# Kernel optimization log

Hardware: AMD Instinct MI355X
Metric: run time of the kernel (lower is better)

The kernel has to match this reference:

```python
import jax, jax.numpy as jnp
import numpy as np

MARGIN = 2.0


def setup_inputs() -> dict:
    key = jax.random.key(0)
    k1, k2 = jax.random.split(key)
    B, D, NUM_CLASSES = 8192, 128, 100
    features = jax.random.normal(k1, (B, D), dtype=jnp.float32)
    labels = jax.random.randint(k2, (B,), 0, NUM_CLASSES, dtype=jnp.int64)
    return {"features": features, "labels": labels}


def reference(features, labels):
    # Vectorized form of the O(B^2) nested-loop contrastive loss.
    B = features.shape[0]
    sq = jnp.sum(features * features, axis=-1)                      # [B]
    # squared pairwise L2 distances via the gram matrix
    d2 = sq[:, None] + sq[None, :] - 2.0 * (features @ features.T)  # [B, B]
    d2 = jnp.maximum(d2, 0.0)

    off_diag = ~jnp.eye(B, dtype=bool)
    same = labels[:, None] == labels[None, :]
    pos_mask = same & off_diag
    neg_mask = (~same) & off_diag

    # positive pairs contribute squared distance
    pos_loss = jnp.sum(jnp.where(pos_mask, d2, 0.0))

    # negative pairs contribute clamp(margin - dist, 0)^2; guard sqrt(0) grads
    d = jnp.sqrt(jnp.where(neg_mask, d2, 1.0))
    hinge = jnp.maximum(MARGIN - d, 0.0)
    neg_loss = jnp.sum(jnp.where(neg_mask, hinge * hinge, 0.0))

    pos_count = jnp.sum(pos_mask)
    total_pairs = jnp.asarray(B * (B - 1), dtype=d2.dtype)
    loss = pos_loss + neg_loss
    # original divides only when positive_pairs > 0
    return jnp.where(pos_count > 0, loss / total_pairs, loss)
```

## Files before the change

### kernel.cpp

```cpp
#include <hip/hip_runtime.h>
#include <hip/hip_bf16.h>


#define BN 8192
#define DD 128
#define NTILES 64
#define NBLOCKS (NTILES * (NTILES + 1) / 2)
#define SQ 26.0f
#define INV_S2 (1.0 / (26.0 * 26.0))
#define INV_S2F (1.0f / (26.0f * 26.0f))
#define D2I_HINGE 2704
#define NCLS 100
#define IMIN ((int)0x80000000)

typedef __attribute__((ext_vector_type(4))) int i32x4;

__global__ __launch_bounds__(256) void prep_kernel(const float* __restrict__ f,
        const int* __restrict__ labels, char* __restrict__ fbp,
        int* __restrict__ normv, int* __restrict__ csum_g) {
    const int tid = threadIdx.x;
    const int p = blockIdx.x;
    __shared__ __align__(16) char ls[16][144];
    __shared__ int lslab[16];

    if (tid < 16) lslab[tid] = labels[p * 16 + tid];

    const int r = tid >> 4;
    const int c = (tid & 15) * 8;
    const float* src = f + ((size_t)p * 16 + r) * DD + c;
    float4 a = *(const float4*)src;
    float4 b = *(const float4*)(src + 4);
    float rv[8] = {a.x, a.y, a.z, a.w, b.x, b.y, b.z, b.w};
    int s = 0;
#pragma unroll
    for (int j = 0; j < 8; j++) {
        int q = __float2int_rn(fminf(fmaxf(rv[j] * SQ, -127.f), 127.f));
        ls[r][c + j] = (char)q;
        s += q * q;
    }
#pragma unroll
    for (int off = 8; off > 0; off >>= 1) s += __shfl_down(s, off, 16);
    if ((tid & 15) == 0) normv[p * 16 + r] = s;
    __syncthreads();

    if (tid < 128) {
        const int ks = tid >> 6, lane = tid & 63;
        const int l15 = lane & 15, quad = lane >> 4;
        i32x4 pack = *(const i32x4*)&ls[l15][ks * 64 + quad * 16];
        *(i32x4*)(fbp + ((size_t)(p * 2 + ks) * 64 + lane) * 16) = pack;
    }

#pragma unroll
    for (int i = 0; i < 8; i++) {
        const int k = tid + i * 256;
        const int row = k >> 7, d = k & 127;
        const int q = (int)(signed char)ls[row][d];
        atomicAdd(&csum_g[lslab[row] * DD + d], q);
    }
}

__global__ __launch_bounds__(256) void pair_kernel(
        const char* __restrict__ fbp, const int* __restrict__ normv,
        const int* __restrict__ labels, float* __restrict__ partial) {
    const int t = blockIdx.x;
    int by = (int)((sqrtf(8.f * (float)t + 1.f) - 1.f) * 0.5f);
    while ((by + 1) * (by + 2) / 2 <= t) by++;
    while (by * (by + 1) / 2 > t) by--;
    const int bx = t - by * (by + 1) / 2;
    const bool diag = (bx == by);

    const int tid = threadIdx.x;
    const int wave = tid >> 6, lane = tid & 63;
    const int wx = wave & 1, wy = wave >> 1;
    const int i0 = bx * 128 + wy * 64;
    const int j0 = by * 128 + wx * 64;
    const int ip = i0 >> 4, jp = j0 >> 4;
    const int l15 = lane & 15, quad = lane >> 4;

    float neg = 0.f;

    if (!(diag && wx < wy)) {
        i32x4 acc4[4][4];
#pragma unroll
        for (int a = 0; a < 4; a++)
#pragma unroll
            for (int b = 0; b < 4; b++) acc4[a][b] = (i32x4){0, 0, 0, 0};

#pragma unroll
        for (int ks = 0; ks < 2; ks++) {
            i32x4 af[4], bg[4];
#pragma unroll
            for (int tt = 0; tt < 4; tt++)
                af[tt] = *(const i32x4*)(fbp +
                    ((size_t)((ip + tt) * 2 + ks) * 64 + lane) * 16);
#pragma unroll
            for (int tt = 0; tt < 4; tt++)
                bg[tt] = *(const i32x4*)(fbp +
                    ((size_t)((jp + tt) * 2 + ks) * 64 + lane) * 16);
#pragma unroll
            for (int m = 0; m < 4; m++)
#pragma unroll
                for (int n = 0; n < 4; n++)
                    acc4[m][n] = __builtin_amdgcn_mfma_i32_16x16x64_i8(
                        af[m], bg[n], acc4[m][n], 0, 0, 0);
        }

        int wn[4];
#pragma unroll
        for (int n = 0; n < 4; n++) wn[n] = normv[j0 + n * 16 + l15];
        int un[4][4];
#pragma unroll
        for (int m = 0; m < 4; m++)
#pragma unroll
            for (int r = 0; r < 4; r++)
                un[m][r] = normv[i0 + m * 16 + quad * 4 + r];

        const bool strict = diag && (wx == wy);
        int amax = IMIN;
        if (!strict) {
#pragma unroll
            for (int m = 0; m < 4; m++)
#pragma unroll
                for (int n = 0; n < 4; n++)
#pragma unroll
                    for (int r = 0; r < 4; r++)
                        amax = max(amax, acc4[m][n][r]);
        } else {
#pragma unroll
            for (int m = 0; m < 4; m++)
#pragma unroll
                for (int n = 0; n < 4; n++)
#pragma unroll
                    for (int r = 0; r < 4; r++) {
                        int il = m * 16 + quad * 4 + r;
                        int jl = n * 16 + l15;
                        amax = max(amax, (il < jl) ? acc4[m][n][r] : IMIN);
                    }
        }
        int umin = un[0][0];
#pragma unroll
        for (int m = 0; m < 4; m++)
#pragma unroll
            for (int r = 0; r < 4; r++) umin = min(umin, un[m][r]);
        int wmin = wn[0];
#pragma unroll
        for (int n = 1; n < 4; n++) wmin = min(wmin, wn[n]);
        const int bound = umin + wmin - 2 * amax;

        if (__any(bound < D2I_HINGE)) {
            int lj[4];
#pragma unroll
            for (int n = 0; n < 4; n++) lj[n] = labels[j0 + n * 16 + l15];
            int li[4][4];
#pragma unroll
            for (int m = 0; m < 4; m++)
#pragma unroll
                for (int r = 0; r < 4; r++)
                    li[m][r] = labels[i0 + m * 16 + quad * 4 + r];
#pragma unroll
            for (int m = 0; m < 4; m++)
#pragma unroll
                for (int n = 0; n < 4; n++)
#pragma unroll
                    for (int r = 0; r < 4; r++) {
                        int il = m * 16 + quad * 4 + r;
                        int jl = n * 16 + l15;
                        bool valid = !strict || (il < jl);
                        int d2i = un[m][r] + wn[n] - 2 * acc4[m][n][r];
                        if (valid && li[m][r] != lj[n] && d2i < D2I_HINGE) {
                            float h = 2.0f - sqrtf((float)d2i * INV_S2F);
                            neg += h * h;
                        }
                    }
        }
    }

#pragma unroll
    for (int off = 32; off > 0; off >>= 1) neg += __shfl_down(neg, off, 64);
    __shared__ float red[4];
    if (lane == 0) red[wave] = neg;
    __syncthreads();
    if (tid == 0) partial[t] = red[0] + red[1] + red[2] + red[3];
}

__global__ __launch_bounds__(256) void reduce_kernel(
        const float* __restrict__ partial, const int* __restrict__ normv,
        const int* __restrict__ labels, const int* __restrict__ csum_g,
        float* __restrict__ out) {
    const int tid = threadIdx.x;
    __shared__ int cnt[NCLS];
    __shared__ int snorm[NCLS];
    __shared__ double posc[NCLS];
    __shared__ float redn[4];

    if (tid < NCLS) { cnt[tid] = 0; snorm[tid] = 0; }
    __syncthreads();
    for (int i = tid; i < BN; i += 256) {
        int l = labels[i];
        atomicAdd(&cnt[l], 1);
        atomicAdd(&snorm[l], normv[i]);
    }
    __syncthreads();
    if (tid < NCLS) {
        long long cc = 0;
        const int* cs = &csum_g[tid * DD];
        for (int d = 0; d < DD; d++) { long long v = cs[d]; cc += v * v; }
        posc[tid] = (double)(2LL * ((long long)cnt[tid] * (long long)snorm[tid] - cc));
    }
    __syncthreads();

    float nsum = 0.f;
    for (int i = tid; i < NBLOCKS; i += 256) nsum += partial[i];
#pragma unroll
    for (int off = 32; off > 0; off >>= 1) nsum += __shfl_down(nsum, off, 64);
    const int lane = tid & 63, w = tid >> 6;
    if (lane == 0) redn[w] = nsum;
    __syncthreads();
    if (tid == 0) {
        double pos = 0.0;
        for (int c = 0; c < NCLS; c++) pos += posc[c];
        double negs = (double)(redn[0] + redn[1] + redn[2] + redn[3]);
        double total = pos * INV_S2 + 2.0 * negs;
        out[0] = (float)(total / 67100672.0);
    }
}

extern "C" void kernel_launch(void* const* d_in, const int* in_sizes, int n_in,
                              void* d_out, int out_size, void* d_ws, size_t ws_size,
                              hipStream_t stream) {
    const float* f = (const float*)d_in[0];
    const int* labels = (const int*)d_in[1];
    float* out = (float*)d_out;

    char* fbp = (char*)d_ws;
    int* normv = (int*)((char*)d_ws + (size_t)BN * DD);
    float* partial = (float*)(normv + BN);
    int* csum_g = (int*)(partial + NBLOCKS);

    hipMemsetAsync(csum_g, 0, NCLS * DD * sizeof(int), stream);
    prep_kernel<<<BN / 16, 256, 0, stream>>>(f, labels, fbp, normv, csum_g);
    pair_kernel<<<NBLOCKS, 256, 0, stream>>>(fbp, normv, labels, partial);
    reduce_kernel<<<1, 256, 0, stream>>>(partial, normv, labels, csum_g, out);
}
```

Measured before the change: 90.31 us.

## Replace per-element atomic class sums with per-class gather kernel

Removes the global atomicAdd scatter of quantized features into per-class sums from the prep kernel, along with the memset. A new kernel, one block per class and half of the batch, gathers that class's row indices and accumulates the quantized values without atomics. It writes two partial sums per class, which the reduce kernel adds together. The change targets the cost of about a million global atomics, but it adds a kernel launch, re-reads features from memory, and caps each class-half at 1024 rows.

New measurement: 94.65 us. 4.8% more time.

```diff
diff --git a/kernel.cpp b/kernel.cpp
--- a/kernel.cpp
+++ b/kernel.cpp
@@ -16,14 +16,10 @@
 typedef __attribute__((ext_vector_type(4))) int i32x4;
 
 __global__ __launch_bounds__(256) void prep_kernel(const float* __restrict__ f,
-        const int* __restrict__ labels, char* __restrict__ fbp,
-        int* __restrict__ normv, int* __restrict__ csum_g) {
+        char* __restrict__ fbp, int* __restrict__ normv) {
     const int tid = threadIdx.x;
     const int p = blockIdx.x;
     __shared__ __align__(16) char ls[16][144];
-    __shared__ int lslab[16];
-
-    if (tid < 16) lslab[tid] = labels[p * 16 + tid];
 
     const int r = tid >> 4;
     const int c = (tid & 15) * 8;
@@ -49,14 +45,40 @@
         i32x4 pack = *(const i32x4*)&ls[l15][ks * 64 + quad * 16];
         *(i32x4*)(fbp + ((size_t)(p * 2 + ks) * 64 + lane) * 16) = pack;
     }
-
-#pragma unroll
-    for (int i = 0; i < 8; i++) {
-        const int k = tid + i * 256;
-        const int row = k >> 7, d = k & 127;
-        const int q = (int)(signed char)ls[row][d];
-        atomicAdd(&csum_g[lslab[row] * DD + d], q);
-    }
+}
+
+__global__ __launch_bounds__(256) void csum_kernel(const float* __restrict__ f,
+        const int* __restrict__ labels, int* __restrict__ csum2) {
+    const int c = blockIdx.x >> 1;
+    const int half = blockIdx.x & 1;
+    const int tid = threadIdx.x;
+    __shared__ int rows[1024];
+    __shared__ int cnt;
+    __shared__ int part[128];
+    if (tid == 0) cnt = 0;
+    __syncthreads();
+
+    const int r0 = half * (BN / 2);
+    for (int i = tid; i < BN / 2; i += 256) {
+        if (labels[r0 + i] == c) {
+            int pidx = atomicAdd(&cnt, 1);
+            if (pidx < 1024) rows[pidx] = r0 + i;
+        }
+    }
+    __syncthreads();
+    const int n = min(cnt, 1024);
+
+    const int d = tid & 127, slot = tid >> 7;
+    int acc = 0;
+    for (int i = slot; i < n; i += 2) {
+        float v = f[(size_t)rows[i] * DD + d];
+        int q = __float2int_rn(fminf(fmaxf(v * SQ, -127.f), 127.f));
+        acc += q;
+    }
+    if (slot == 1) part[d] = acc;
+    __syncthreads();
+    if (slot == 0)
+        csum2[((size_t)half * NCLS + c) * DD + d] = acc + part[d];
 }
 
 __global__ __launch_bounds__(256) void pair_kernel(
@@ -185,7 +207,7 @@
 
 __global__ __launch_bounds__(256) void reduce_kernel(
         const float* __restrict__ partial, const int* __restrict__ normv,
-        const int* __restrict__ labels, const int* __restrict__ csum_g,
+        const int* __restrict__ labels, const int* __restrict__ csum2,
         float* __restrict__ out) {
     const int tid = threadIdx.x;
     __shared__ int cnt[NCLS];
@@ -203,8 +225,12 @@
     __syncthreads();
     if (tid < NCLS) {
         long long cc = 0;
-        const int* cs = &csum_g[tid * DD];
-        for (int d = 0; d < DD; d++) { long long v = cs[d]; cc += v * v; }
+        const int* cs0 = &csum2[(size_t)tid * DD];
+        const int* cs1 = &csum2[((size_t)NCLS + tid) * DD];
+        for (int d = 0; d < DD; d++) {
+            long long v = (long long)(cs0[d] + cs1[d]);
+            cc += v * v;
+        }
         posc[tid] = (double)(2LL * ((long long)cnt[tid] * (long long)snorm[tid] - cc));
     }
     __syncthreads();
@@ -235,10 +261,10 @@
     char* fbp = (char*)d_ws;
     int* normv = (int*)((char*)d_ws + (size_t)BN * DD);
     float* partial = (float*)(normv + BN);
-    int* csum_g = (int*)(partial + NBLOCKS);
-
-    hipMemsetAsync(csum_g, 0, NCLS * DD * sizeof(int), stream);
-    prep_kernel<<<BN / 16, 256, 0, stream>>>(f, labels, fbp, normv, csum_g);
+    int* csum2 = (int*)(partial + NBLOCKS);
+
+    prep_kernel<<<BN / 16, 256, 0, stream>>>(f, fbp, normv);
+    csum_kernel<<<2 * NCLS, 256, 0, stream>>>(f, labels, csum2);
     pair_kernel<<<NBLOCKS, 256, 0, stream>>>(fbp, normv, labels, partial);
-    reduce_kernel<<<1, 256, 0, stream>>>(partial, normv, labels, csum_g, out);
-}
+    reduce_kernel<<<1, 256, 0, stream>>>(partial, normv, labels, csum2, out);
+}
```
